# Performance work log

Measured on AMD Instinct MI355X. Metric: run time of the kernel, lower is better.

The kernel has to match this reference:

```python
import jax, jax.numpy as jnp
import numpy as np

BN_EPS = 1e-5


def setup_inputs() -> dict:
    key = jax.random.key(0)
    ks = jax.random.split(key, 4)
    B, N, D = 8, 8192, 256
    outD = 256
    s = 1.0 / np.sqrt(D)
    return {
        "feature": jax.random.normal(ks[0], (B, N, D), dtype=jnp.float32),
        "W_qk": jax.random.normal(ks[1], (2, D, D), dtype=jnp.float32) * s,
        "b_qk": jnp.zeros((2, D), dtype=jnp.float32),
        "W_v": jax.random.normal(ks[2], (D, outD), dtype=jnp.float32) * s,
        "b_v": jnp.zeros((outD,), dtype=jnp.float32),
        "gamma": jnp.ones((D,), dtype=jnp.float32),
        "beta": jnp.zeros((D,), dtype=jnp.float32),
    }


def reference(feature, W_qk, b_qk, W_v, b_v, gamma, beta):
    # QK: [B, 2, N, D]
    QK = jnp.einsum("bnd,kde->bkne", feature, W_qk) + b_qk[None, :, None, :]
    # value: [B, N, outD]
    value = jnp.einsum("bnd,de->bne", feature, W_v) + b_v
    query = QK[:, 0]  # [B, N, D]
    key = QK[:, 1]    # [B, N, D]
    # softmax over the sequence axis (dim=1), per (batch, channel)
    sm = jax.nn.softmax(key, axis=1)
    # lambda context: softmax^T @ value -> [B, D, outD]
    lam = jnp.einsum("bnd,bne->bde", sm, value)
    # BatchNorm1d(featureDim) in training mode: channel axis = D (axis 1),
    # stats over (batch, spatial) = axes (0, 2); biased variance as torch uses.
    mean = jnp.mean(lam, axis=(0, 2), keepdims=True)
    var = jnp.var(lam, axis=(0, 2), keepdims=True)
    bn = (lam - mean) * jax.lax.rsqrt(var + BN_EPS)
    bn = bn * gamma[None, :, None] + beta[None, :, None]
    # result: query @ BN -> [B, N, outD]
    return jnp.einsum("bnd,bde->bne", query, bn)
```

## Files before the change

### kernel.cpp

```cpp
#include <hip/hip_runtime.h>

typedef unsigned short u16;
typedef __bf16 bf16x8 __attribute__((ext_vector_type(8)));
typedef float f32x4 __attribute__((ext_vector_type(4)));

#define LOG2E 1.44269504088896f

__device__ inline u16 f2b(float f) {
    unsigned u = __float_as_uint(f);
    u += 0x7fff + ((u >> 16) & 1);
    return (u16)(u >> 16);
}
__device__ inline float b2f(u16 u) { return __uint_as_float(((unsigned)u) << 16); }
__device__ inline unsigned pk2(float a, float b) {
    return (unsigned)f2b(a) | ((unsigned)f2b(b) << 16);
}
__device__ inline uint4 pack8(float4 a, float4 b) {
    return uint4{pk2(a.x, a.y), pk2(a.z, a.w), pk2(b.x, b.y), pk2(b.z, b.w)};
}
__device__ inline f32x4 mfma_bf16(uint4 a, uint4 b, f32x4 c) {
    return __builtin_amdgcn_mfma_f32_16x16x32_bf16(
        __builtin_bit_cast(bf16x8, a), __builtin_bit_cast(bf16x8, b), c, 0, 0, 0);
}
__device__ inline void ld16(const u16* g, u16* l) {
    __builtin_amdgcn_global_load_lds(
        (const __attribute__((address_space(1))) unsigned int*)g,
        (__attribute__((address_space(3))) unsigned int*)l, 16, 0, 0);
}


__global__ __launch_bounds__(256) void prep_w(const float* __restrict__ Wqk,
                                              const float* __restrict__ Wv,
                                              u16* __restrict__ WkT,
                                              u16* __restrict__ WvT,
                                              u16* __restrict__ Wqb) {
    int idx = blockIdx.x * 256 + threadIdx.x;
    int which = idx >> 16;
    int i = (idx >> 8) & 255;
    int j = idx & 255;
    if (which == 0)
        WkT[i * 256 + j] = f2b(Wqk[65536 + j * 256 + i]);
    else if (which == 1)
        WvT[i * 256 + j] = f2b(Wv[j * 256 + i]);
    else
        Wqb[i * 256 + j] = f2b(Wqk[i * 256 + j]);
}

__global__ __launch_bounds__(256, 2) void gemm_kv(const float* __restrict__ A,
                                                  const u16* __restrict__ BtK,
                                                  const u16* __restrict__ BtV,
                                                  const float* __restrict__ biasK,
                                                  const float* __restrict__ biasV,
                                                  u16* __restrict__ KT,
                                                  u16* __restrict__ VT) {
    __shared__ __align__(16) u16 lds[36864];

    const int t = threadIdx.x;
    const int r0 = blockIdx.x * 64;
    const int w = t >> 6, lane = t & 63, l15 = lane & 15, q = lane >> 4;
    const int sq = ((lane & 3) ^ ((lane >> 3) & 3)) * 8;
    const int qs = (q ^ ((l15 >> 1) & 3)) * 8;
    const int awoff = (t >> 2) * 32 + sq;
    const int brr = t >> 2;

    f32x4 accK[4][4], accV[4][4];
#pragma unroll
    for (int rt = 0; rt < 4; ++rt)
#pragma unroll
        for (int ct = 0; ct < 4; ++ct) {
            accK[rt][ct] = f32x4{0.f, 0.f, 0.f, 0.f};
            accV[rt][ct] = f32x4{0.f, 0.f, 0.f, 0.f};
        }

    const float* Arow = A + (long)(r0 + brr) * 256 + (t & 3) * 8;
    float4 p0 = ((const float4*)Arow)[0], p1 = ((const float4*)Arow)[1];
    float4 c0_ = *(const float4*)(Arow + 32), c1_ = *(const float4*)(Arow + 36);
    float4 d0_ = *(const float4*)(Arow + 64), d1_ = *(const float4*)(Arow + 68);

    {
        u16* dK = lds + 4096 + w * 512;
#pragma unroll
        for (int j = 0; j < 4; ++j) {
            int br = j * 64 + brr;
            ld16(BtK + br * 256 + sq, dK + j * 2048);
            ld16(BtV + br * 256 + sq, dK + 8192 + j * 2048);
        }
    }
    *(uint4*)(lds + awoff) = pack8(p0, p1);
    __syncthreads();

#pragma unroll
    for (int t8 = 0; t8 < 8; ++t8) {
        const int cur = t8 & 1;
        if (t8 < 7) {
            const int k0 = (t8 + 1) * 32;
            u16* dK = lds + 4096 + (cur ^ 1) * 16384 + w * 512;
#pragma unroll
            for (int j = 0; j < 4; ++j) {
                int br = j * 64 + brr;
                ld16(BtK + br * 256 + k0 + sq, dK + j * 2048);
                ld16(BtV + br * 256 + k0 + sq, dK + 8192 + j * 2048);
            }
            *(uint4*)(lds + (cur ^ 1) * 2048 + awoff) = pack8(c0_, c1_);
            c0_ = d0_; c1_ = d1_;
            if (t8 < 5) {
                d0_ = *(const float4*)(Arow + (t8 + 3) * 32);
                d1_ = *(const float4*)(Arow + (t8 + 3) * 32 + 4);
            }
        }
        const u16* Asc = lds + cur * 2048;
        const u16* Bc = lds + 4096 + cur * 16384;
        uint4 af[4];
#pragma unroll
        for (int rt = 0; rt < 4; ++rt)
            af[rt] = *(const uint4*)(Asc + (rt * 16 + l15) * 32 + qs);
#pragma unroll
        for (int ct = 0; ct < 4; ++ct) {
            const int bo = (w * 64 + ct * 16 + l15) * 32 + qs;
            uint4 bK = *(const uint4*)(Bc + bo);
            uint4 bV = *(const uint4*)(Bc + 8192 + bo);
#pragma unroll
            for (int rt = 0; rt < 4; ++rt) {
                accK[rt][ct] = mfma_bf16(af[rt], bK, accK[rt][ct]);
                accV[rt][ct] = mfma_bf16(af[rt], bV, accV[rt][ct]);
            }
        }
        __syncthreads();
    }

    const int bb = r0 >> 13, n0 = r0 & 8191;
    u16* Ct = lds;
#pragma unroll
    for (int pass = 0; pass < 2; ++pass) {
        const f32x4(*acc)[4] = pass ? accV : accK;
        const float* bias = pass ? biasV : biasK;
        u16* CT = pass ? VT : KT;
#pragma unroll
        for (int ct = 0; ct < 4; ++ct) {
            const int col = w * 64 + ct * 16 + l15;
            const float bv = bias[col];
#pragma unroll
            for (int rt = 0; rt < 4; ++rt) {
                ushort4 pk;
                pk.x = f2b(acc[rt][ct][0] + bv);
                pk.y = f2b(acc[rt][ct][1] + bv);
                pk.z = f2b(acc[rt][ct][2] + bv);
                pk.w = f2b(acc[rt][ct][3] + bv);
                *(ushort4*)&Ct[col * 72 + rt * 16 + q * 4] = pk;
            }
        }
        __syncthreads();
        long off = ((long)bb * 256 + t) * 8192 + n0;
#pragma unroll
        for (int j = 0; j < 8; ++j)
            *(uint4*)(CT + off + j * 8) = *(const uint4*)&Ct[t * 72 + j * 8];
        __syncthreads();
    }
}

__global__ __launch_bounds__(256, 3) void gemm_out(const float* __restrict__ A,
                                                   const u16* __restrict__ WfoldT,
                                                   const float* __restrict__ outb,
                                                   float* __restrict__ C) {
    __shared__ __align__(16) u16 lds[20480];
    const int t = threadIdx.x;
    const int r0 = blockIdx.x * 64;
    const int bb = r0 >> 13;
    const int w = t >> 6, lane = t & 63, l15 = lane & 15, q = lane >> 4;
    const int sq = ((lane & 3) ^ ((lane >> 3) & 3)) * 8;
    const int qs = (q ^ ((l15 >> 1) & 3)) * 8;
    const int awoff = (t >> 2) * 32 + sq;
    const int brr = t >> 2;
    const u16* Bt = WfoldT + (long)bb * 65536;

    f32x4 acc[4][4];
#pragma unroll
    for (int rt = 0; rt < 4; ++rt)
#pragma unroll
        for (int ct = 0; ct < 4; ++ct) acc[rt][ct] = f32x4{0.f, 0.f, 0.f, 0.f};

    const float* Arow = A + (long)(r0 + brr) * 256 + (t & 3) * 8;
    float4 p0 = ((const float4*)Arow)[0], p1 = ((const float4*)Arow)[1];
    float4 c0_ = *(const float4*)(Arow + 32), c1_ = *(const float4*)(Arow + 36);
    float4 d0_ = *(const float4*)(Arow + 64), d1_ = *(const float4*)(Arow + 68);

    {
        u16* dB = lds + 4096 + w * 512;
#pragma unroll
        for (int j = 0; j < 4; ++j)
            ld16(Bt + (j * 64 + brr) * 256 + sq, dB + j * 2048);
    }
    *(uint4*)(lds + awoff) = pack8(p0, p1);
    __syncthreads();

#pragma unroll
    for (int t8 = 0; t8 < 8; ++t8) {
        const int cur = t8 & 1;
        if (t8 < 7) {
            const int k0 = (t8 + 1) * 32;
            u16* dB = lds + 4096 + (cur ^ 1) * 8192 + w * 512;
#pragma unroll
            for (int j = 0; j < 4; ++j)
                ld16(Bt + (j * 64 + brr) * 256 + k0 + sq, dB + j * 2048);
            *(uint4*)(lds + (cur ^ 1) * 2048 + awoff) = pack8(c0_, c1_);
            c0_ = d0_; c1_ = d1_;
            if (t8 < 5) {
                d0_ = *(const float4*)(Arow + (t8 + 3) * 32);
                d1_ = *(const float4*)(Arow + (t8 + 3) * 32 + 4);
            }
        }
        const u16* Asc = lds + cur * 2048;
        const u16* Bc = lds + 4096 + cur * 8192;
        uint4 af[4];
#pragma unroll
        for (int rt = 0; rt < 4; ++rt)
            af[rt] = *(const uint4*)(Asc + (rt * 16 + l15) * 32 + qs);
#pragma unroll
        for (int ct = 0; ct < 4; ++ct) {
            uint4 bf = *(const uint4*)(Bc + (w * 64 + ct * 16 + l15) * 32 + qs);
#pragma unroll
            for (int rt = 0; rt < 4; ++rt)
                acc[rt][ct] = mfma_bf16(af[rt], bf, acc[rt][ct]);
        }
        __syncthreads();
    }

#pragma unroll
    for (int ct = 0; ct < 4; ++ct) {
        const int col = w * 64 + ct * 16 + l15;
        const float bv = outb[bb * 256 + col];
#pragma unroll
        for (int rt = 0; rt < 4; ++rt) {
#pragma unroll
            for (int r = 0; r < 4; ++r) {
                int row = r0 + rt * 16 + q * 4 + r;
                C[(long)row * 256 + col] = acc[rt][ct][r] + bv;
            }
        }
    }
}

__global__ __launch_bounds__(256, 2) void gemm_splitk(const u16* __restrict__ VT,
                                                      const u16* __restrict__ PT,
                                                      float* __restrict__ lamP,
                                                      int chunk) {
    __shared__ __align__(16) u16 lds[16384];
    const int t = threadIdx.x;
    const int r0 = blockIdx.x * 128;
    const int c0 = blockIdx.y * 128;
    const int s = blockIdx.z;
    const int bb = blockIdx.x >> 1;
    const long n0 = (long)s * chunk;
    const int w = t >> 6, lane = t & 63, l15 = lane & 15, q = lane >> 4;
    const int sq = ((lane & 3) ^ ((lane >> 3) & 3)) * 8;
    const int qs = (q ^ ((l15 >> 1) & 3)) * 8;
    const int brr = t >> 2;

    const u16* Abase = VT + (long)r0 * 8192 + n0;
    const u16* Bbase = PT + ((long)bb * 256 + c0) * 8192 + n0;

    f32x4 acc[8][2];
#pragma unroll
    for (int rt = 0; rt < 8; ++rt) {
        acc[rt][0] = f32x4{0.f, 0.f, 0.f, 0.f};
        acc[rt][1] = f32x4{0.f, 0.f, 0.f, 0.f};
    }

    {
        u16* dA = lds + w * 512;
#pragma unroll
        for (int j = 0; j < 2; ++j) {
            int br = j * 64 + brr;
            ld16(Abase + (long)br * 8192 + sq, dA + j * 2048);
            ld16(Bbase + (long)br * 8192 + sq, dA + 4096 + j * 2048);
        }
    }
    __syncthreads();

    const int nk = chunk >> 5;
    for (int ks = 0; ks < nk; ++ks) {
        const int cur = ks & 1;
        if (ks + 1 < nk) {
            const int k0 = (ks + 1) * 32;
            u16* dA = lds + (cur ^ 1) * 8192 + w * 512;
#pragma unroll
            for (int j = 0; j < 2; ++j) {
                int br = j * 64 + brr;
                ld16(Abase + (long)br * 8192 + k0 + sq, dA + j * 2048);
                ld16(Bbase + (long)br * 8192 + k0 + sq, dA + 4096 + j * 2048);
            }
        }
        const u16* Asc = lds + cur * 8192;
        const u16* Bsc = Asc + 4096;
        const int bo = (w * 32 + l15) * 32 + qs;
        uint4 bf0 = *(const uint4*)(Bsc + bo);
        uint4 bf1 = *(const uint4*)(Bsc + 512 + bo);
#pragma unroll
        for (int rt = 0; rt < 8; ++rt) {
            uint4 af = *(const uint4*)(Asc + (rt * 16 + l15) * 32 + qs);
            acc[rt][0] = mfma_bf16(af, bf0, acc[rt][0]);
            acc[rt][1] = mfma_bf16(af, bf1, acc[rt][1]);
        }
        __syncthreads();
    }

    float* outp = lamP + (long)s * 524288;
#pragma unroll
    for (int rt = 0; rt < 8; ++rt)
#pragma unroll
        for (int ct = 0; ct < 2; ++ct) {
            const int col = c0 + w * 32 + ct * 16 + l15;
#pragma unroll
            for (int r = 0; r < 4; ++r)
                outp[(long)(r0 + rt * 16 + q * 4 + r) * 256 + col] = acc[rt][ct][r];
        }
}

__global__ __launch_bounds__(256) void reduce_lam(const float* __restrict__ lamP,
                                                  float* __restrict__ lamT, int S) {
    int i = blockIdx.x * 256 + threadIdx.x;
    float4 v = ((const float4*)lamP)[i];
    for (int s = 1; s < S; ++s) {
        float4 p = ((const float4*)(lamP + (long)s * 524288))[i];
        v.x += p.x; v.y += p.y; v.z += p.z; v.w += p.w;
    }
    ((float4*)lamT)[i] = v;
}

__global__ __launch_bounds__(256, 4) void gemm_fold(const u16* __restrict__ Abn,
                                                    const u16* __restrict__ Wqb,
                                                    u16* __restrict__ WfoldT) {
    __shared__ __align__(16) u16 lds[4096];
    u16* As = lds;
    u16* Bs = lds + 2048;

    const int t = threadIdx.x;
    const int r0 = blockIdx.x * 64;
    const int c0 = blockIdx.y * 64;
    const int w = t >> 6, lane = t & 63, l15 = lane & 15, q = lane >> 4;

    f32x4 acc[4];
#pragma unroll
    for (int c = 0; c < 4; ++c) acc[c] = f32x4{0.f, 0.f, 0.f, 0.f};

    const int br = t >> 2;
    const int bk = (t & 3) * 8;

    for (int k0 = 0; k0 < 256; k0 += 32) {
        ld16(Abn + (long)(r0 + br) * 256 + k0 + bk, As + w * 512);
        ld16(Wqb + (long)(c0 + br) * 256 + k0 + bk, Bs + w * 512);
        __syncthreads();
        uint4 af = *(const uint4*)(As + (w * 16 + l15) * 32 + q * 8);
#pragma unroll
        for (int c = 0; c < 4; ++c) {
            uint4 bf = *(const uint4*)(Bs + (c * 16 + l15) * 32 + q * 8);
            acc[c] = mfma_bf16(af, bf, acc[c]);
        }
        __syncthreads();
    }

#pragma unroll
    for (int c = 0; c < 4; ++c) {
        int col = c0 + c * 16 + l15;
#pragma unroll
        for (int r = 0; r < 4; ++r) {
            int row = r0 + w * 16 + q * 4 + r;
            WfoldT[(long)row * 256 + col] = f2b(acc[c][r]);
        }
    }
}

__global__ __launch_bounds__(64) void softmax_rows(u16* __restrict__ KT) {
    const int row = blockIdx.x;
    const int lane = threadIdx.x;
    u16* p = KT + (long)row * 8192;

    uint4 buf[16];
#pragma unroll
    for (int i = 0; i < 16; ++i) buf[i] = *(const uint4*)(p + (i * 64 + lane) * 8);

    float m = -1e30f;
#pragma unroll
    for (int i = 0; i < 16; ++i) {
        const unsigned* u = (const unsigned*)&buf[i];
#pragma unroll
        for (int j = 0; j < 4; ++j) {
            m = fmaxf(m, fmaxf(b2f((u16)(u[j] & 0xffff)), b2f((u16)(u[j] >> 16))));
        }
    }
#pragma unroll
    for (int s = 32; s > 0; s >>= 1) m = fmaxf(m, __shfl_xor(m, s, 64));

    float sum = 0.f;
#pragma unroll
    for (int i = 0; i < 16; ++i) {
        const unsigned* u = (const unsigned*)&buf[i];
#pragma unroll
        for (int j = 0; j < 4; ++j) {
            sum += exp2f((b2f((u16)(u[j] & 0xffff)) - m) * LOG2E);
            sum += exp2f((b2f((u16)(u[j] >> 16)) - m) * LOG2E);
        }
    }
#pragma unroll
    for (int s = 32; s > 0; s >>= 1) sum += __shfl_xor(sum, s, 64);
    float rl = 1.0f / sum;

#pragma unroll
    for (int i = 0; i < 16; ++i) {
        unsigned* u = (unsigned*)&buf[i];
#pragma unroll
        for (int j = 0; j < 4; ++j) {
            float a = exp2f((b2f((u16)(u[j] & 0xffff)) - m) * LOG2E) * rl;
            float b = exp2f((b2f((u16)(u[j] >> 16)) - m) * LOG2E) * rl;
            u[j] = (unsigned)f2b(a) | ((unsigned)f2b(b) << 16);
        }
        *(uint4*)(p + (i * 64 + lane) * 8) = buf[i];
    }
}

__global__ __launch_bounds__(256) void bn_kernel(const float* __restrict__ lamT,
                                                 const float* __restrict__ gamma,
                                                 const float* __restrict__ beta,
                                                 u16* __restrict__ bnT) {
    const int d = blockIdx.x;
    const int t = threadIdx.x;
    float vals[8];
    float s = 0.f, ss = 0.f;
#pragma unroll
    for (int i = 0; i < 8; ++i) {
        float v = lamT[(long)(i * 256 + t) * 256 + d];
        vals[i] = v;
        s += v;
        ss += v * v;
    }
#pragma unroll
    for (int sh = 32; sh > 0; sh >>= 1) {
        s += __shfl_xor(s, sh, 64);
        ss += __shfl_xor(ss, sh, 64);
    }
    __shared__ float red[8];
    int w = t >> 6;
    if ((t & 63) == 0) {
        red[w] = s;
        red[w + 4] = ss;
    }
    __syncthreads();
    s = red[0] + red[1] + red[2] + red[3];
    ss = red[4] + red[5] + red[6] + red[7];
    float mean = s * (1.f / 2048.f);
    float var = ss * (1.f / 2048.f) - mean * mean;
    float scale = gamma[d] * rsqrtf(var + 1e-5f);
    float shift = beta[d] - mean * scale;
#pragma unroll
    for (int i = 0; i < 8; ++i)
        bnT[(long)(i * 256 + t) * 256 + d] = f2b(vals[i] * scale + shift);
}

__global__ __launch_bounds__(256) void outb_kernel(const float* __restrict__ bq,
                                                   const u16* __restrict__ bnT,
                                                   float* __restrict__ outb) {
    int b = blockIdx.x, e = threadIdx.x;
    const u16* rowp = bnT + ((long)b * 256 + e) * 256;
    float s = 0.f;
    for (int dd = 0; dd < 256; ++dd) s += bq[dd] * b2f(rowp[dd]);
    outb[b * 256 + e] = s;
}

extern "C" void kernel_launch(void* const* d_in, const int* in_sizes, int n_in,
                              void* d_out, int out_size, void* d_ws, size_t ws_size,
                              hipStream_t stream) {
    const float* feat = (const float*)d_in[0];
    const float* W_qk = (const float*)d_in[1];
    const float* b_qk = (const float*)d_in[2];
    const float* W_v = (const float*)d_in[3];
    const float* b_v = (const float*)d_in[4];
    const float* gamma = (const float*)d_in[5];
    const float* beta = (const float*)d_in[6];
    float* out = (float*)d_out;

    char* ws = (char*)d_ws;
    u16* KT = (u16*)(ws);
    u16* VT = (u16*)(ws + 33554432);
    u16* WkT = (u16*)(ws + 67108864);
    u16* WvT = (u16*)(ws + 67239936);
    u16* Wqb = (u16*)(ws + 67371008);
    const size_t base = 67502080;
    float* lamP = (float*)(ws + base);
    size_t avail = (ws_size > base) ? ws_size - base : 0;
    int S = (avail >= 16u * 2097152u) ? 16
          : (avail >= 8u * 2097152u) ? 8
          : (avail >= 4u * 2097152u) ? 4 : 2;
    float* lamT = (float*)ws;
    u16* bnT = (u16*)(ws + 2097152);
    u16* WfoldT = (u16*)(ws + 3145728);
    float* outb = (float*)(ws + 4194304);

    prep_w<<<768, 256, 0, stream>>>(W_qk, W_v, WkT, WvT, Wqb);
    gemm_kv<<<1024, 256, 0, stream>>>(feat, WkT, WvT, b_qk + 256, b_v, KT, VT);
    softmax_rows<<<2048, 64, 0, stream>>>(KT);
    gemm_splitk<<<dim3(16, 2, S), 256, 0, stream>>>(VT, KT, lamP, 8192 / S);
    reduce_lam<<<512, 256, 0, stream>>>(lamP, lamT, S);
    bn_kernel<<<256, 256, 0, stream>>>(lamT, gamma, beta, bnT);
    outb_kernel<<<8, 256, 0, stream>>>(b_qk, bnT, outb);
    gemm_fold<<<dim3(32, 4), 256, 0, stream>>>(bnT, Wqb, WfoldT);
    gemm_out<<<1024, 256, 0, stream>>>(feat, WfoldT, outb, out);
}
```

Measured before the change: 252.4 us.

## Fuse softmax stats into KV GEMM epilogue and apply exp in split-K GEMM

Removes the separate softmax_rows pass over K. The KV GEMM epilogue now computes per-tile online max and sum-exp partials, a small stats2 kernel merges them into a log-sum-exp table, and the split-K GEMM applies exp(k - lse) to its B fragments as it loads them. K/V are also stored in a tiled [b][ntile][channel][32] layout so the split-K loads are contiguous. This saves a full read-modify-write of the 32MB K tensor, at the cost of extra exp work inside the GEMM inner loop and one extra small kernel.

```diff
diff --git a/kernel.cpp b/kernel.cpp
--- a/kernel.cpp
+++ b/kernel.cpp
@@ -26,6 +26,21 @@
     __builtin_amdgcn_global_load_lds(
         (const __attribute__((address_space(1))) unsigned int*)g,
         (__attribute__((address_space(3))) unsigned int*)l, 16, 0, 0);
+}
+__device__ inline uint4 expfrag(uint4 v, float nc) {
+    float e[8];
+#pragma unroll
+    for (int i = 0; i < 4; ++i) {
+        unsigned u = ((const unsigned*)&v)[i];
+        e[2 * i] = exp2f(fmaf(b2f((u16)(u & 0xffff)), LOG2E, nc));
+        e[2 * i + 1] = exp2f(fmaf(b2f((u16)(u >> 16)), LOG2E, nc));
+    }
+    uint4 r;
+    asm("v_cvt_pk_bf16_f32 %0, %1, %2" : "=v"(r.x) : "v"(e[0]), "v"(e[1]));
+    asm("v_cvt_pk_bf16_f32 %0, %1, %2" : "=v"(r.y) : "v"(e[2]), "v"(e[3]));
+    asm("v_cvt_pk_bf16_f32 %0, %1, %2" : "=v"(r.z) : "v"(e[4]), "v"(e[5]));
+    asm("v_cvt_pk_bf16_f32 %0, %1, %2" : "=v"(r.w) : "v"(e[6]), "v"(e[7]));
+    return r;
 }
 
 
@@ -52,7 +67,8 @@
                                                   const float* __restrict__ biasK,
                                                   const float* __restrict__ biasV,
                                                   u16* __restrict__ KT,
-                                                  u16* __restrict__ VT) {
+                                                  u16* __restrict__ VT,
+                                                  float* __restrict__ partial) {
     __shared__ __align__(16) u16 lds[36864];
 
     const int t = threadIdx.x;
@@ -128,7 +144,9 @@
         __syncthreads();
     }
 
-    const int bb = r0 >> 13, n0 = r0 & 8191;
+    const int bb = r0 >> 13;
+    const int nt0 = (r0 & 8191) >> 5;
+    const int nch = nt0 >> 1;
     u16* Ct = lds;
 #pragma unroll
     for (int pass = 0; pass < 2; ++pass) {
@@ -139,6 +157,7 @@
         for (int ct = 0; ct < 4; ++ct) {
             const int col = w * 64 + ct * 16 + l15;
             const float bv = bias[col];
+            ushort4 pks[4];
 #pragma unroll
             for (int rt = 0; rt < 4; ++rt) {
                 ushort4 pk;
@@ -146,16 +165,63 @@
                 pk.y = f2b(acc[rt][ct][1] + bv);
                 pk.z = f2b(acc[rt][ct][2] + bv);
                 pk.w = f2b(acc[rt][ct][3] + bv);
+                pks[rt] = pk;
                 *(ushort4*)&Ct[col * 72 + rt * 16 + q * 4] = pk;
             }
-        }
-        __syncthreads();
-        long off = ((long)bb * 256 + t) * 8192 + n0;
-#pragma unroll
-        for (int j = 0; j < 8; ++j)
-            *(uint4*)(CT + off + j * 8) = *(const uint4*)&Ct[t * 72 + j * 8];
-        __syncthreads();
-    }
+            if (pass == 0) {
+                float zm = -1e30f;
+#pragma unroll
+                for (int rt = 0; rt < 4; ++rt)
+                    zm = fmaxf(zm,
+                               fmaxf(fmaxf(b2f(pks[rt].x), b2f(pks[rt].y)),
+                                     fmaxf(b2f(pks[rt].z), b2f(pks[rt].w))));
+                zm = fmaxf(zm, __shfl_xor(zm, 16, 64));
+                zm = fmaxf(zm, __shfl_xor(zm, 32, 64));
+                zm *= LOG2E;
+                float zs = 0.f;
+#pragma unroll
+                for (int rt = 0; rt < 4; ++rt) {
+                    zs += exp2f(fmaf(b2f(pks[rt].x), LOG2E, -zm));
+                    zs += exp2f(fmaf(b2f(pks[rt].y), LOG2E, -zm));
+                    zs += exp2f(fmaf(b2f(pks[rt].z), LOG2E, -zm));
+                    zs += exp2f(fmaf(b2f(pks[rt].w), LOG2E, -zm));
+                }
+                zs += __shfl_xor(zs, 16, 64);
+                zs += __shfl_xor(zs, 32, 64);
+                if (q == 0) {
+                    float* pp =
+                        partial + (((long)(bb * 128 + nch)) * 256 + col) * 2;
+                    pp[0] = zm;
+                    pp[1] = zs;
+                }
+            }
+        }
+        __syncthreads();
+        {
+            const long tb = (((long)(bb * 256 + nt0)) * 256 + t) * 32;
+#pragma unroll
+            for (int j2 = 0; j2 < 2; ++j2)
+#pragma unroll
+                for (int g = 0; g < 4; ++g)
+                    *(uint4*)(CT + tb + j2 * 8192 + g * 8) =
+                        *(const uint4*)&Ct[t * 72 + j2 * 32 + g * 8];
+        }
+        __syncthreads();
+    }
+}
+
+__global__ __launch_bounds__(256) void stats2(const float* __restrict__ partial,
+                                              float* __restrict__ ctab) {
+    const int b = blockIdx.x, d = threadIdx.x;
+    float M = -1e30f;
+    for (int i = 0; i < 128; ++i)
+        M = fmaxf(M, partial[(((long)(b * 128 + i)) * 256 + d) * 2]);
+    float S = 0.f;
+    for (int i = 0; i < 128; ++i) {
+        const float* pp = partial + (((long)(b * 128 + i)) * 256 + d) * 2;
+        S += pp[1] * exp2f(pp[0] - M);
+    }
+    ctab[b * 256 + d] = M + log2f(S);
 }
 
 __global__ __launch_bounds__(256, 3) void gemm_out(const float* __restrict__ A,
@@ -231,17 +297,17 @@
         const float bv = outb[bb * 256 + col];
 #pragma unroll
         for (int rt = 0; rt < 4; ++rt) {
-#pragma unroll
-            for (int r = 0; r < 4; ++r) {
-                int row = r0 + rt * 16 + q * 4 + r;
-                C[(long)row * 256 + col] = acc[rt][ct][r] + bv;
-            }
+            const long rbase = r0 + rt * 16 + q * 4;
+#pragma unroll
+            for (int r = 0; r < 4; ++r)
+                C[(rbase + r) * 256 + col] = acc[rt][ct][r] + bv;
         }
     }
 }
 
 __global__ __launch_bounds__(256, 2) void gemm_splitk(const u16* __restrict__ VT,
-                                                      const u16* __restrict__ PT,
+                                                      const u16* __restrict__ KT,
+                                                      const float* __restrict__ ctab,
                                                       float* __restrict__ lamP,
                                                       int chunk) {
     __shared__ __align__(16) u16 lds[16384];
@@ -249,15 +315,18 @@
     const int r0 = blockIdx.x * 128;
     const int c0 = blockIdx.y * 128;
     const int s = blockIdx.z;
-    const int bb = blockIdx.x >> 1;
-    const long n0 = (long)s * chunk;
+    const int bA = r0 >> 8, e0 = r0 & 255;
     const int w = t >> 6, lane = t & 63, l15 = lane & 15, q = lane >> 4;
     const int sq = ((lane & 3) ^ ((lane >> 3) & 3)) * 8;
     const int qs = (q ^ ((l15 >> 1) & 3)) * 8;
     const int brr = t >> 2;
 
-    const u16* Abase = VT + (long)r0 * 8192 + n0;
-    const u16* Bbase = PT + ((long)bb * 256 + c0) * 8192 + n0;
+    const int nt_base = (int)(((long)s * chunk) >> 5);
+    const u16* Abase = VT + (((long)bA * 256 + nt_base) * 256 + e0) * 32;
+    const u16* Bbase = KT + (((long)bA * 256 + nt_base) * 256 + c0) * 32;
+
+    const float nc0 = -ctab[bA * 256 + c0 + w * 32 + l15];
+    const float nc1 = -ctab[bA * 256 + c0 + w * 32 + 16 + l15];
 
     f32x4 acc[8][2];
 #pragma unroll
@@ -271,8 +340,8 @@
 #pragma unroll
         for (int j = 0; j < 2; ++j) {
             int br = j * 64 + brr;
-            ld16(Abase + (long)br * 8192 + sq, dA + j * 2048);
-            ld16(Bbase + (long)br * 8192 + sq, dA + 4096 + j * 2048);
+            ld16(Abase + br * 32 + sq, dA + j * 2048);
+            ld16(Bbase + br * 32 + sq, dA + 4096 + j * 2048);
         }
     }
     __syncthreads();
@@ -281,20 +350,20 @@
     for (int ks = 0; ks < nk; ++ks) {
         const int cur = ks & 1;
         if (ks + 1 < nk) {
-            const int k0 = (ks + 1) * 32;
+            const long toff = (long)(ks + 1) * 8192;
             u16* dA = lds + (cur ^ 1) * 8192 + w * 512;
 #pragma unroll
             for (int j = 0; j < 2; ++j) {
                 int br = j * 64 + brr;
-                ld16(Abase + (long)br * 8192 + k0 + sq, dA + j * 2048);
-                ld16(Bbase + (long)br * 8192 + k0 + sq, dA + 4096 + j * 2048);
+                ld16(Abase + toff + br * 32 + sq, dA + j * 2048);
+                ld16(Bbase + toff + br * 32 + sq, dA + 4096 + j * 2048);
             }
         }
         const u16* Asc = lds + cur * 8192;
         const u16* Bsc = Asc + 4096;
         const int bo = (w * 32 + l15) * 32 + qs;
-        uint4 bf0 = *(const uint4*)(Bsc + bo);
-        uint4 bf1 = *(const uint4*)(Bsc + 512 + bo);
+        uint4 bf0 = expfrag(*(const uint4*)(Bsc + bo), nc0);
+        uint4 bf1 = expfrag(*(const uint4*)(Bsc + 512 + bo), nc1);
 #pragma unroll
         for (int rt = 0; rt < 8; ++rt) {
             uint4 af = *(const uint4*)(Asc + (rt * 16 + l15) * 32 + qs);
@@ -312,7 +381,8 @@
             const int col = c0 + w * 32 + ct * 16 + l15;
 #pragma unroll
             for (int r = 0; r < 4; ++r)
-                outp[(long)(r0 + rt * 16 + q * 4 + r) * 256 + col] = acc[rt][ct][r];
+                outp[(long)(r0 + rt * 16 + q * 4 + r) * 256 + col] =
+                    acc[rt][ct][r];
         }
 }
 
@@ -367,54 +437,6 @@
             int row = r0 + w * 16 + q * 4 + r;
             WfoldT[(long)row * 256 + col] = f2b(acc[c][r]);
         }
-    }
-}
-
-__global__ __launch_bounds__(64) void softmax_rows(u16* __restrict__ KT) {
-    const int row = blockIdx.x;
-    const int lane = threadIdx.x;
-    u16* p = KT + (long)row * 8192;
-
-    uint4 buf[16];
-#pragma unroll
-    for (int i = 0; i < 16; ++i) buf[i] = *(const uint4*)(p + (i * 64 + lane) * 8);
-
-    float m = -1e30f;
-#pragma unroll
-    for (int i = 0; i < 16; ++i) {
-        const unsigned* u = (const unsigned*)&buf[i];
-#pragma unroll
-        for (int j = 0; j < 4; ++j) {
-            m = fmaxf(m, fmaxf(b2f((u16)(u[j] & 0xffff)), b2f((u16)(u[j] >> 16))));
-        }
-    }
-#pragma unroll
-    for (int s = 32; s > 0; s >>= 1) m = fmaxf(m, __shfl_xor(m, s, 64));
-
-    float sum = 0.f;
-#pragma unroll
-    for (int i = 0; i < 16; ++i) {
-        const unsigned* u = (const unsigned*)&buf[i];
-#pragma unroll
-        for (int j = 0; j < 4; ++j) {
-            sum += exp2f((b2f((u16)(u[j] & 0xffff)) - m) * LOG2E);
-            sum += exp2f((b2f((u16)(u[j] >> 16)) - m) * LOG2E);
-        }
-    }
-#pragma unroll
-    for (int s = 32; s > 0; s >>= 1) sum += __shfl_xor(sum, s, 64);
-    float rl = 1.0f / sum;
-
-#pragma unroll
-    for (int i = 0; i < 16; ++i) {
-        unsigned* u = (unsigned*)&buf[i];
-#pragma unroll
-        for (int j = 0; j < 4; ++j) {
-            float a = exp2f((b2f((u16)(u[j] & 0xffff)) - m) * LOG2E) * rl;
-            float b = exp2f((b2f((u16)(u[j] >> 16)) - m) * LOG2E) * rl;
-            u[j] = (unsigned)f2b(a) | ((unsigned)f2b(b) << 16);
-        }
-        *(uint4*)(p + (i * 64 + lane) * 8) = buf[i];
     }
 }
 
@@ -484,7 +506,9 @@
     u16* WkT = (u16*)(ws + 67108864);
     u16* WvT = (u16*)(ws + 67239936);
     u16* Wqb = (u16*)(ws + 67371008);
-    const size_t base = 67502080;
+    float* partial = (float*)(ws + 67502080);
+    float* ctab = (float*)(ws + 69599232);
+    const size_t base = 69607424;
     float* lamP = (float*)(ws + base);
     size_t avail = (ws_size > base) ? ws_size - base : 0;
     int S = (avail >= 16u * 2097152u) ? 16
@@ -496,9 +520,10 @@
     float* outb = (float*)(ws + 4194304);
 
     prep_w<<<768, 256, 0, stream>>>(W_qk, W_v, WkT, WvT, Wqb);
-    gemm_kv<<<1024, 256, 0, stream>>>(feat, WkT, WvT, b_qk + 256, b_v, KT, VT);
-    softmax_rows<<<2048, 64, 0, stream>>>(KT);
-    gemm_splitk<<<dim3(16, 2, S), 256, 0, stream>>>(VT, KT, lamP, 8192 / S);
+    gemm_kv<<<1024, 256, 0, stream>>>(feat, WkT, WvT, b_qk + 256, b_v, KT, VT,
+                                      partial);
+    stats2<<<8, 256, 0, stream>>>(partial, ctab);
+    gemm_splitk<<<dim3(16, 2, S), 256, 0, stream>>>(VT, KT, ctab, lamP, 8192 / S);
     reduce_lam<<<512, 256, 0, stream>>>(lamP, lamT, S);
     bn_kernel<<<256, 256, 0, stream>>>(lamT, gamma, beta, bnT);
     outb_kernel<<<8, 256, 0, stream>>>(b_qk, bnT, outb);
```

New measurement: 272.8 us. +8.1%, slower.
